# Performance work log

Measured on AMD Instinct MI355X. Metric: run time of the kernel, lower is better.

The kernel has to match this reference:

```python
import jax, jax.numpy as jnp
import numpy as np

N = 50000          # nodes
E = 800000         # edges
F_IN, H, OUT = 512, 256, 2
BN_EPS = 1e-5


def setup_inputs() -> dict:
    key = jax.random.key(0)
    ks = jax.random.split(key, 10)
    x = jax.random.normal(ks[0], (N, F_IN), jnp.float32)
    edge_index = jax.random.randint(ks[1], (2, E), 0, N, dtype=jnp.int64)
    edge_weight = jax.random.uniform(ks[2], (E,), jnp.float32)

    def lin(k, fan_in, fan_out):
        return jax.random.normal(k, (fan_in, fan_out), jnp.float32) / np.sqrt(fan_in).astype(np.float32)

    W1, b1 = lin(ks[3], F_IN, H), jnp.zeros((H,), jnp.float32)
    W2, b2 = lin(ks[4], H, H), jnp.zeros((H,), jnp.float32)
    W3, b3 = lin(ks[5], H, OUT), jnp.zeros((OUT,), jnp.float32)
    # BatchNorm1d affine params + running stats (eval mode)
    g1, be1 = jnp.ones((H,), jnp.float32), jnp.zeros((H,), jnp.float32)
    m1 = 0.1 * jax.random.normal(ks[6], (H,), jnp.float32)
    v1 = jax.random.uniform(ks[7], (H,), jnp.float32, 0.5, 1.5)
    g2, be2 = jnp.ones((H,), jnp.float32), jnp.zeros((H,), jnp.float32)
    m2 = 0.1 * jax.random.normal(ks[8], (H,), jnp.float32)
    v2 = jax.random.uniform(ks[9], (H,), jnp.float32, 0.5, 1.5)
    return {"x": x, "edge_index": edge_index, "edge_weight": edge_weight,
            "W1": W1, "b1": b1, "g1": g1, "be1": be1, "m1": m1, "v1": v1,
            "W2": W2, "b2": b2, "g2": g2, "be2": be2, "m2": m2, "v2": v2,
            "W3": W3, "b3": b3}


def gcn_conv(x, row, col, w, W, b):
    # PyG GCNConv (eval): h = x @ W; out[col] += norm * h[row]; + b
    # row/col/w already include self-loops with weight 1.
    n = x.shape[0]
    h = x @ W                                      # [N, out]
    deg = jax.ops.segment_sum(w, col, num_segments=n)
    dinv = jnp.where(deg > 0, jax.lax.rsqrt(deg), 0.0)
    norm = dinv[row] * w * dinv[col]               # [E+N]
    out = jax.ops.segment_sum(h[row] * norm[:, None], col, num_segments=n)
    return out + b


def batchnorm_eval(x, g, be, m, v):
    return (x - m) * jax.lax.rsqrt(v + BN_EPS) * g + be


def reference(x, edge_index, edge_weight, W1, b1, g1, be1, m1, v1,
              W2, b2, g2, be2, m2, v2, W3, b3):
    n = x.shape[0]
    loops = jnp.arange(n, dtype=edge_index.dtype)
    row = jnp.concatenate([edge_index[0], loops])
    col = jnp.concatenate([edge_index[1], loops])
    w = jnp.concatenate([edge_weight, jnp.ones((n,), x.dtype)])

    h = jax.nn.relu(batchnorm_eval(gcn_conv(x, row, col, w, W1, b1), g1, be1, m1, v1))
    h = jax.nn.relu(batchnorm_eval(gcn_conv(h, row, col, w, W2, b2), g2, be2, m2, v2))
    return gcn_conv(h, row, col, w, W3, b3)
```

## Files before the change

kernel.cpp:

```cpp
#include <hip/hip_runtime.h>
#include <stdint.h>

#define F_IN 512
#define HF 256
#define OUT_F 2
#define BN_EPS 1e-5f
#define SCAN_B 256
#define LDSTR 36

typedef __attribute__((ext_vector_type(8))) short bf16x8;
typedef __attribute__((ext_vector_type(4))) float f32x4;

__device__ inline float bf2f(unsigned short u) {
    union { float f; uint32_t i; } v; v.i = ((uint32_t)u) << 16; return v.f;
}
__device__ inline unsigned short f2bf(float f) {
    union { float f; uint32_t i; } v; v.f = f;
    uint32_t r = v.i + 0x7FFFu + ((v.i >> 16) & 1u);
    return (unsigned short)(r >> 16);
}

__global__ void count_conv_kernel(const int* __restrict__ col,
                                  const float* __restrict__ w,
                                  unsigned long long* __restrict__ packed,
                                  const float* __restrict__ x,
                                  unsigned short* __restrict__ xbf,
                                  const float* __restrict__ W1, unsigned short* __restrict__ W1t,
                                  const float* __restrict__ W2, unsigned short* __restrict__ W2t,
                                  unsigned short* __restrict__ xbf_pad,
                                  unsigned short* __restrict__ bufa_pad,
                                  int e, int nchunk, int padx, int pada) {
    int tid = blockIdx.x * blockDim.x + threadIdx.x;
    const int stride = gridDim.x * blockDim.x;
    if (tid < e) {
        unsigned long long add = (1ULL << 40)
            | (unsigned long long)__float2uint_rn(w[tid] * 1048576.0f);
        atomicAdd(&packed[col[tid]], add);
    }
    const float4* x4 = (const float4*)x;
    for (int c = tid; c < nchunk; c += stride) {
        float4 f0 = x4[2 * c];
        float4 f1 = x4[2 * c + 1];
        bf16x8 v;
        v[0] = (short)f2bf(f0.x); v[1] = (short)f2bf(f0.y);
        v[2] = (short)f2bf(f0.z); v[3] = (short)f2bf(f0.w);
        v[4] = (short)f2bf(f1.x); v[5] = (short)f2bf(f1.y);
        v[6] = (short)f2bf(f1.z); v[7] = (short)f2bf(f1.w);
        *(bf16x8*)(xbf + (size_t)c * 8) = v;
    }
    for (int j = tid; j < F_IN * HF; j += stride) {
        int nn = j >> 9, k = j & (F_IN - 1);
        W1t[j] = f2bf(W1[(size_t)k * HF + nn]);
    }
    for (int j = tid; j < HF * HF; j += stride) {
        int nn = j >> 8, k = j & (HF - 1);
        W2t[j] = f2bf(W2[(size_t)k * HF + nn]);
    }
    for (int j = tid; j < padx; j += stride) xbf_pad[j] = 0;
    for (int j = tid; j < pada; j += stride) bufa_pad[j] = 0;
}

__global__ void scan1_kernel(const unsigned long long* __restrict__ packed,
                             int* __restrict__ local, int* __restrict__ blocksum, int n) {
    __shared__ int tmp[SCAN_B];
    int i = blockIdx.x * SCAN_B + threadIdx.x;
    int v = (i < n) ? (int)(packed[i] >> 40) : 0;
    tmp[threadIdx.x] = v;
    __syncthreads();
    for (int off = 1; off < SCAN_B; off <<= 1) {
        int t = 0;
        if ((int)threadIdx.x >= off) t = tmp[threadIdx.x - off];
        __syncthreads();
        if ((int)threadIdx.x >= off) tmp[threadIdx.x] += t;
        __syncthreads();
    }
    if (i < n) local[i] = tmp[threadIdx.x] - v;
    if (threadIdx.x == SCAN_B - 1) blocksum[blockIdx.x] = tmp[SCAN_B - 1];
}

__global__ void scan3_dinv_kernel(int* __restrict__ csr_ptr, int* __restrict__ cursor,
                                  const int* __restrict__ blocksum,
                                  const unsigned long long* __restrict__ packed,
                                  float* __restrict__ dinv, int n, int e, int nb) {
    __shared__ int red[SCAN_B];
    int t = threadIdx.x;
    red[t] = (t < nb && t < (int)blockIdx.x) ? blocksum[t] : 0;
    __syncthreads();
    for (int off = SCAN_B / 2; off > 0; off >>= 1) {
        if (t < off) red[t] += red[t + off];
        __syncthreads();
    }
    int prefix = red[0];
    int i = blockIdx.x * SCAN_B + t;
    if (i < n) {
        int val = csr_ptr[i] + prefix;
        csr_ptr[i] = val;
        cursor[i] = val;
        float deg = 1.0f + (float)(packed[i] & 0xFFFFFFFFFFULL) * (1.0f / 1048576.0f);
        dinv[i] = rsqrtf(deg);
    }
    if (i == 0) csr_ptr[n] = e;
}

__device__ __forceinline__
void gemm_body(const unsigned short* __restrict__ A,
               const unsigned short* __restrict__ Bt,
               unsigned short* __restrict__ C, int K, int mblk, int nblk,
               unsigned short (*As)[128 * LDSTR], unsigned short (*Bs)[128 * LDSTR]) {
    const int tid  = threadIdx.x;
    const int lane = tid & 63;
    const int wv   = tid >> 6;
    const int wrow = wv >> 1, wcol = wv & 1;
    const int m0 = mblk * 128;
    const int n0 = nblk * 128;

    const int sr = tid >> 2;
    const int sc = (tid & 3) * 8;

    const unsigned short* pa0 = A + (size_t)(m0 + sr) * K + sc;
    const unsigned short* pa1 = A + (size_t)(m0 + sr + 64) * K + sc;
    const unsigned short* pb0 = Bt + (size_t)(n0 + sr) * K + sc;
    const unsigned short* pb1 = Bt + (size_t)(n0 + sr + 64) * K + sc;

    f32x4 zero4 = {0.0f, 0.0f, 0.0f, 0.0f};
    f32x4 acc[4][4];
    #pragma unroll
    for (int i = 0; i < 4; ++i)
        #pragma unroll
        for (int j = 0; j < 4; ++j) acc[i][j] = zero4;

    const int q8 = (lane >> 4) * 8;
    const int ml = lane & 15;

    bf16x8 va0 = *(const bf16x8*)pa0;
    bf16x8 va1 = *(const bf16x8*)pa1;
    bf16x8 vb0 = *(const bf16x8*)pb0;
    bf16x8 vb1 = *(const bf16x8*)pb1;

    const int nsteps = K >> 5;
    for (int s = 0; s < nsteps; ++s) {
        const int buf = s & 1;
        *(bf16x8*)&As[buf][sr * LDSTR + sc]        = va0;
        *(bf16x8*)&As[buf][(sr + 64) * LDSTR + sc] = va1;
        *(bf16x8*)&Bs[buf][sr * LDSTR + sc]        = vb0;
        *(bf16x8*)&Bs[buf][(sr + 64) * LDSTR + sc] = vb1;
        __syncthreads();
        if (s + 1 < nsteps) {
            int off = (s + 1) * 32;
            va0 = *(const bf16x8*)(pa0 + off);
            va1 = *(const bf16x8*)(pa1 + off);
            vb0 = *(const bf16x8*)(pb0 + off);
            vb1 = *(const bf16x8*)(pb1 + off);
        }
        bf16x8 af[4], bfr[4];
        #pragma unroll
        for (int i = 0; i < 4; ++i)
            af[i] = *(const bf16x8*)&As[buf][(wrow * 64 + i * 16 + ml) * LDSTR + q8];
        #pragma unroll
        for (int j = 0; j < 4; ++j)
            bfr[j] = *(const bf16x8*)&Bs[buf][(wcol * 64 + j * 16 + ml) * LDSTR + q8];
        #pragma unroll
        for (int i = 0; i < 4; ++i)
            #pragma unroll
            for (int j = 0; j < 4; ++j)
                acc[i][j] = __builtin_amdgcn_mfma_f32_16x16x32_bf16(af[i], bfr[j], acc[i][j], 0, 0, 0);
    }

    const int q4 = (lane >> 4) * 4;
    #pragma unroll
    for (int i = 0; i < 4; ++i) {
        #pragma unroll
        for (int j = 0; j < 4; ++j) {
            #pragma unroll
            for (int rg = 0; rg < 4; ++rg) {
                int r = m0 + wrow * 64 + i * 16 + q4 + rg;
                int c = n0 + wcol * 64 + j * 16 + ml;
                C[(size_t)r * HF + c] = f2bf(acc[i][j][rg]);
            }
        }
    }
}

__global__ __launch_bounds__(256)
void fill_gemm1_kernel(const int* __restrict__ row, const int* __restrict__ col,
                       const float* __restrict__ w, const float* __restrict__ dinv,
                       int* __restrict__ cursor, int2* __restrict__ csr_edge, int e,
                       const unsigned short* __restrict__ A,
                       const unsigned short* __restrict__ Bt,
                       unsigned short* __restrict__ C, int nfill) {
    __shared__ unsigned short As[2][128 * LDSTR];
    __shared__ unsigned short Bs[2][128 * LDSTR];
    int bid = blockIdx.x;
    if (bid < nfill) {
        int i = bid * 256 + (int)threadIdx.x;
        if (i < e) {
            int r = row[i], c = col[i];
            int pos = atomicAdd(&cursor[c], 1);
            float nrm = dinv[r] * w[i] * dinv[c];
            csr_edge[pos] = make_int2(r, __float_as_int(nrm));
        }
    } else {
        int gb = bid - nfill;
        gemm_body(A, Bt, C, F_IN, gb >> 1, gb & 1, As, Bs);
    }
}

__global__ __launch_bounds__(256)
void gemm_kernel(const unsigned short* __restrict__ A,
                 const unsigned short* __restrict__ Bt,
                 unsigned short* __restrict__ C, int K) {
    __shared__ unsigned short As[2][128 * LDSTR];
    __shared__ unsigned short Bs[2][128 * LDSTR];
    gemm_body(A, Bt, C, K, blockIdx.x, blockIdx.y, As, Bs);
}

template<int FINAL>
__global__ void agg_kernel(const unsigned short* __restrict__ h,
                           const int* __restrict__ ptr,
                           const int2* __restrict__ edge,
                           const float* __restrict__ dinv,
                           const float* __restrict__ b, const float* __restrict__ g,
                           const float* __restrict__ be, const float* __restrict__ m,
                           const float* __restrict__ v,
                           unsigned short* __restrict__ out,
                           const float* __restrict__ W3, float* __restrict__ h3, int n) {
    int wid  = (blockIdx.x * blockDim.x + threadIdx.x) >> 6;
    int lane = threadIdx.x & 63;
    if (wid >= n) return;
    int p0 = ptr[wid], p1 = ptr[wid + 1];
    const int fo = lane * 4;
    float a0 = 0.f, a1 = 0.f, a2 = 0.f, a3 = 0.f;

    const int cnt = p1 - p0;
    const int nb  = cnt >> 3;

    int2 edC[8], edN[8];
    ushort4 hvC[8];

    if (nb > 0) {
        #pragma unroll
        for (int k = 0; k < 8; ++k) edC[k] = edge[p0 + k];
        if (nb > 1) {
            #pragma unroll
            for (int k = 0; k < 8; ++k) edN[k] = edge[p0 + 8 + k];
        }
        #pragma unroll
        for (int k = 0; k < 8; ++k)
            hvC[k] = *(const ushort4*)(h + (size_t)edC[k].x * HF + fo);

        for (int bb = 0; bb < nb; ++bb) {
            ushort4 hvN[8];
            int2 edN2[8];
            if (bb + 1 < nb) {
                if (bb + 2 < nb) {
                    int pp = p0 + (bb + 2) * 8;
                    #pragma unroll
                    for (int k = 0; k < 8; ++k) edN2[k] = edge[pp + k];
                }
                #pragma unroll
                for (int k = 0; k < 8; ++k)
                    hvN[k] = *(const ushort4*)(h + (size_t)edN[k].x * HF + fo);
            }
            #pragma unroll
            for (int k = 0; k < 8; ++k) {
                float nw = __int_as_float(edC[k].y);
                a0 += nw * bf2f(hvC[k].x);
                a1 += nw * bf2f(hvC[k].y);
                a2 += nw * bf2f(hvC[k].z);
                a3 += nw * bf2f(hvC[k].w);
            }
            #pragma unroll
            for (int k = 0; k < 8; ++k) { edC[k] = edN[k]; edN[k] = edN2[k]; hvC[k] = hvN[k]; }
        }
    }
    const int pend = p0 + nb * 8;
    if (pend < p1) {
        int2 ed[8];
        float wv[8];
        #pragma unroll
        for (int k = 0; k < 8; ++k) {
            int idx = pend + k < p1 ? pend + k : p1 - 1;
            ed[k] = edge[idx];
            wv[k] = (pend + k < p1) ? __int_as_float(ed[k].y) : 0.0f;
        }
        ushort4 hv[8];
        #pragma unroll
        for (int k = 0; k < 8; ++k)
            hv[k] = *(const ushort4*)(h + (size_t)ed[k].x * HF + fo);
        #pragma unroll
        for (int k = 0; k < 8; ++k) {
            a0 += wv[k] * bf2f(hv[k].x);
            a1 += wv[k] * bf2f(hv[k].y);
            a2 += wv[k] * bf2f(hv[k].z);
            a3 += wv[k] * bf2f(hv[k].w);
        }
    }
    float s = dinv[wid];
    float sl = s * s;
    ushort4 hv = *(const ushort4*)(h + (size_t)wid * HF + fo);
    a0 += sl * bf2f(hv.x);
    a1 += sl * bf2f(hv.y);
    a2 += sl * bf2f(hv.z);
    a3 += sl * bf2f(hv.w);

    float4 bb  = *(const float4*)(b + fo);
    float4 gg  = *(const float4*)(g + fo);
    float4 bee = *(const float4*)(be + fo);
    float4 mm  = *(const float4*)(m + fo);
    float4 vv  = *(const float4*)(v + fo);
    float f0 = fmaxf((a0 + bb.x - mm.x) * rsqrtf(vv.x + BN_EPS) * gg.x + bee.x, 0.f);
    float f1 = fmaxf((a1 + bb.y - mm.y) * rsqrtf(vv.y + BN_EPS) * gg.y + bee.y, 0.f);
    float f2 = fmaxf((a2 + bb.z - mm.z) * rsqrtf(vv.z + BN_EPS) * gg.z + bee.z, 0.f);
    float f3 = fmaxf((a3 + bb.w - mm.w) * rsqrtf(vv.w + BN_EPS) * gg.w + bee.w, 0.f);

    if (!FINAL) {
        ushort4 o;
        o.x = f2bf(f0); o.y = f2bf(f1); o.z = f2bf(f2); o.w = f2bf(f3);
        *(ushort4*)(out + (size_t)wid * HF + fo) = o;
    } else {
        float4 w0 = *(const float4*)(W3 + fo * 2);
        float4 w1 = *(const float4*)(W3 + fo * 2 + 4);
        float s0 = f0 * w0.x + f1 * w0.z + f2 * w1.x + f3 * w1.z;
        float s1 = f0 * w0.y + f1 * w0.w + f2 * w1.y + f3 * w1.w;
        #pragma unroll
        for (int o = 32; o > 0; o >>= 1) {
            s0 += __shfl_down(s0, o, 64);
            s1 += __shfl_down(s1, o, 64);
        }
        if (lane == 0) {
            h3[wid * 2 + 0] = s0;
            h3[wid * 2 + 1] = s1;
        }
    }
}

__global__ void out_kernel(const float* __restrict__ h3,
                           const int* __restrict__ ptr, const int2* __restrict__ edge,
                           const float* __restrict__ dinv,
                           const float* __restrict__ b3, float* __restrict__ out, int n) {
    int i = blockIdx.x * blockDim.x + threadIdx.x;
    if (i >= n) return;
    int p0 = ptr[i], p1 = ptr[i + 1];
    float a0 = 0.f, a1 = 0.f;
    for (int p = p0; p < p1; p += 4) {
        #pragma unroll
        for (int k = 0; k < 4; ++k) {
            int idx = p + k < p1 ? p + k : p1 - 1;
            int2 e = edge[idx];
            float nw = (p + k < p1) ? __int_as_float(e.y) : 0.0f;
            float2 u = *(const float2*)(h3 + 2 * e.x);
            a0 += nw * u.x;
            a1 += nw * u.y;
        }
    }
    float s = dinv[i];
    float sl = s * s;
    out[2 * i + 0] = a0 + sl * h3[2 * i + 0] + b3[0];
    out[2 * i + 1] = a1 + sl * h3[2 * i + 1] + b3[1];
}

static inline char* align16(char* p) {
    return (char*)(((uintptr_t)p + 15) & ~(uintptr_t)15);
}

extern "C" void kernel_launch(void* const* d_in, const int* in_sizes, int n_in,
                              void* d_out, int out_size, void* d_ws, size_t ws_size,
                              hipStream_t stream) {
    const float* x   = (const float*)d_in[0];
    const int*   ei  = (const int*)d_in[1];
    const float* ew  = (const float*)d_in[2];
    const float* W1  = (const float*)d_in[3];
    const float* b1  = (const float*)d_in[4];
    const float* g1  = (const float*)d_in[5];
    const float* be1 = (const float*)d_in[6];
    const float* m1  = (const float*)d_in[7];
    const float* v1  = (const float*)d_in[8];
    const float* W2  = (const float*)d_in[9];
    const float* b2  = (const float*)d_in[10];
    const float* g2  = (const float*)d_in[11];
    const float* be2 = (const float*)d_in[12];
    const float* m2  = (const float*)d_in[13];
    const float* v2  = (const float*)d_in[14];
    const float* W3  = (const float*)d_in[15];
    const float* b3  = (const float*)d_in[16];

    const int N  = in_sizes[0] / F_IN;
    const int E  = in_sizes[2];
    const int MP = (N + 127) & ~127;
    const int* row = ei;
    const int* col = ei + E;

    char* wsb = (char*)d_ws;
    unsigned long long* packed = (unsigned long long*)wsb; wsb = align16(wsb + (size_t)N * 8);
    float* dinv     = (float*)wsb;          wsb = align16(wsb + (size_t)N * 4);
    int*   csr_ptr  = (int*)wsb;            wsb = align16(wsb + (size_t)(N + 1) * 4);
    int*   cursor   = (int*)wsb;            wsb = align16(wsb + (size_t)N * 4);
    int*   blocksum = (int*)wsb;            wsb = align16(wsb + (size_t)SCAN_B * 4);
    int2*  csr_edge = (int2*)wsb;           wsb = align16(wsb + (size_t)E * 8);
    unsigned short* W1t = (unsigned short*)wsb;  wsb = align16(wsb + (size_t)F_IN * HF * 2);
    unsigned short* W2t = (unsigned short*)wsb;  wsb = align16(wsb + (size_t)HF * HF * 2);
    unsigned short* xbf  = (unsigned short*)wsb; wsb = align16(wsb + (size_t)MP * F_IN * 2);
    unsigned short* bufh = (unsigned short*)wsb; wsb = align16(wsb + (size_t)MP * HF * 2);
    unsigned short* bufa = (unsigned short*)wsb; wsb = align16(wsb + (size_t)MP * HF * 2);
    float* h3 = (float*)wsb;                wsb = align16(wsb + (size_t)N * OUT_F * 4);
    float* outf = (float*)d_out;

    const int TB = 256;
    const int nscan = (N + SCAN_B - 1) / SCAN_B;
    const int padx = (MP - N) * F_IN;
    const int pada = (MP - N) * HF;
    const int ncc = (E + TB - 1) / TB;
    const int nchunk = (N * F_IN) / 8;
    const int nfill = (E + TB - 1) / TB;
    const int ngemm = (MP / 128) * 2;

    hipMemsetAsync(packed, 0, (size_t)N * 8, stream);

    count_conv_kernel<<<ncc, TB, 0, stream>>>(
        col, ew, packed, x, xbf, W1, W1t, W2, W2t,
        xbf + (size_t)N * F_IN, bufa + (size_t)N * HF, E, nchunk, padx, pada);

    scan1_kernel<<<nscan, SCAN_B, 0, stream>>>(packed, csr_ptr, blocksum, N);
    scan3_dinv_kernel<<<nscan, SCAN_B, 0, stream>>>(csr_ptr, cursor, blocksum, packed, dinv, N, E, nscan);

    fill_gemm1_kernel<<<nfill + ngemm, TB, 0, stream>>>(
        row, col, ew, dinv, cursor, csr_edge, E, xbf, W1t, bufh, nfill);

    agg_kernel<0><<<((size_t)N * 64 + TB - 1) / TB, TB, 0, stream>>>(
        bufh, csr_ptr, csr_edge, dinv, b1, g1, be1, m1, v1, bufa, nullptr, nullptr, N);

    dim3 ggrid(MP / 128, HF / 128);
    gemm_kernel<<<ggrid, TB, 0, stream>>>(bufa, W2t, bufh, HF);

    agg_kernel<1><<<((size_t)N * 64 + TB - 1) / TB, TB, 0, stream>>>(
        bufh, csr_ptr, csr_edge, dinv, b2, g2, be2, m2, v2, nullptr, W3, h3, N);

    out_kernel<<<(N + TB - 1) / TB, TB, 0, stream>>>(h3, csr_ptr, csr_edge, dinv, b3, outf, N);
}
```

Before: 533.3 us.

## Fuse two-pass scan into one kernel with grid barrier; cap fill blocks

Merges the block-local scan and prefix-add/dinv kernels into a single kernel. Each block publishes its partial sum and then spin-waits on an atomic counter until all blocks have done so. This removes one kernel launch and the csr_ptr round-trip, but depends on all ~196 blocks being co-resident to avoid deadlock. Separately, the CSR fill part of the fused fill+GEMM1 kernel now uses 512 blocks with a grid-stride loop instead of one block per 256 edges, which shrinks the grid.

```diff
diff --git a/kernel.cpp b/kernel.cpp
--- a/kernel.cpp
+++ b/kernel.cpp
@@ -60,40 +60,44 @@
     for (int j = tid; j < pada; j += stride) bufa_pad[j] = 0;
 }
 
-__global__ void scan1_kernel(const unsigned long long* __restrict__ packed,
-                             int* __restrict__ local, int* __restrict__ blocksum, int n) {
+__global__ void scan_kernel(const unsigned long long* __restrict__ packed,
+                            int* __restrict__ csr_ptr, int* __restrict__ cursor,
+                            float* __restrict__ dinv,
+                            int* __restrict__ partial, int* __restrict__ counter,
+                            int n, int e, int nb) {
     __shared__ int tmp[SCAN_B];
-    int i = blockIdx.x * SCAN_B + threadIdx.x;
+    const int tid = threadIdx.x;
+    const int bid = blockIdx.x;
+    int i = bid * SCAN_B + tid;
     int v = (i < n) ? (int)(packed[i] >> 40) : 0;
-    tmp[threadIdx.x] = v;
+    tmp[tid] = v;
     __syncthreads();
     for (int off = 1; off < SCAN_B; off <<= 1) {
         int t = 0;
-        if ((int)threadIdx.x >= off) t = tmp[threadIdx.x - off];
+        if (tid >= off) t = tmp[tid - off];
         __syncthreads();
-        if ((int)threadIdx.x >= off) tmp[threadIdx.x] += t;
+        if (tid >= off) tmp[tid] += t;
         __syncthreads();
     }
-    if (i < n) local[i] = tmp[threadIdx.x] - v;
-    if (threadIdx.x == SCAN_B - 1) blocksum[blockIdx.x] = tmp[SCAN_B - 1];
-}
-
-__global__ void scan3_dinv_kernel(int* __restrict__ csr_ptr, int* __restrict__ cursor,
-                                  const int* __restrict__ blocksum,
-                                  const unsigned long long* __restrict__ packed,
-                                  float* __restrict__ dinv, int n, int e, int nb) {
-    __shared__ int red[SCAN_B];
-    int t = threadIdx.x;
-    red[t] = (t < nb && t < (int)blockIdx.x) ? blocksum[t] : 0;
+    int excl = tmp[tid] - v;
+    if (tid == SCAN_B - 1) {
+        partial[bid] = tmp[SCAN_B - 1];
+        __threadfence();
+        atomicAdd(counter, 1);
+    }
+    if (tid == 0) {
+        while (__hip_atomic_load(counter, __ATOMIC_ACQUIRE, __HIP_MEMORY_SCOPE_AGENT) < nb) {}
+    }
+    __syncthreads();
+    tmp[tid] = (tid < nb && tid < bid) ? partial[tid] : 0;
     __syncthreads();
     for (int off = SCAN_B / 2; off > 0; off >>= 1) {
-        if (t < off) red[t] += red[t + off];
+        if (tid < off) tmp[tid] += tmp[tid + off];
         __syncthreads();
     }
-    int prefix = red[0];
-    int i = blockIdx.x * SCAN_B + t;
+    int prefix = tmp[0];
     if (i < n) {
-        int val = csr_ptr[i] + prefix;
+        int val = excl + prefix;
         csr_ptr[i] = val;
         cursor[i] = val;
         float deg = 1.0f + (float)(packed[i] & 0xFFFFFFFFFFULL) * (1.0f / 1048576.0f);
@@ -192,8 +196,8 @@
     __shared__ unsigned short Bs[2][128 * LDSTR];
     int bid = blockIdx.x;
     if (bid < nfill) {
-        int i = bid * 256 + (int)threadIdx.x;
-        if (i < e) {
+        const int stride = nfill * 256;
+        for (int i = bid * 256 + (int)threadIdx.x; i < e; i += stride) {
             int r = row[i], c = col[i];
             int pos = atomicAdd(&cursor[c], 1);
             float nrm = dinv[r] * w[i] * dinv[c];
@@ -391,11 +395,12 @@
     const int* col = ei + E;
 
     char* wsb = (char*)d_ws;
-    unsigned long long* packed = (unsigned long long*)wsb; wsb = align16(wsb + (size_t)N * 8);
+    unsigned long long* packed = (unsigned long long*)wsb; wsb = align16(wsb + (size_t)(N + 2) * 8);
+    int* counter    = (int*)(packed + N);
     float* dinv     = (float*)wsb;          wsb = align16(wsb + (size_t)N * 4);
     int*   csr_ptr  = (int*)wsb;            wsb = align16(wsb + (size_t)(N + 1) * 4);
     int*   cursor   = (int*)wsb;            wsb = align16(wsb + (size_t)N * 4);
-    int*   blocksum = (int*)wsb;            wsb = align16(wsb + (size_t)SCAN_B * 4);
+    int*   partial  = (int*)wsb;            wsb = align16(wsb + (size_t)SCAN_B * 4);
     int2*  csr_edge = (int2*)wsb;           wsb = align16(wsb + (size_t)E * 8);
     unsigned short* W1t = (unsigned short*)wsb;  wsb = align16(wsb + (size_t)F_IN * HF * 2);
     unsigned short* W2t = (unsigned short*)wsb;  wsb = align16(wsb + (size_t)HF * HF * 2);
@@ -411,17 +416,17 @@
     const int pada = (MP - N) * HF;
     const int ncc = (E + TB - 1) / TB;
     const int nchunk = (N * F_IN) / 8;
-    const int nfill = (E + TB - 1) / TB;
+    const int nfill = 512;
     const int ngemm = (MP / 128) * 2;
 
-    hipMemsetAsync(packed, 0, (size_t)N * 8, stream);
+    hipMemsetAsync(packed, 0, (size_t)(N + 2) * 8, stream);
 
     count_conv_kernel<<<ncc, TB, 0, stream>>>(
         col, ew, packed, x, xbf, W1, W1t, W2, W2t,
         xbf + (size_t)N * F_IN, bufa + (size_t)N * HF, E, nchunk, padx, pada);
 
-    scan1_kernel<<<nscan, SCAN_B, 0, stream>>>(packed, csr_ptr, blocksum, N);
-    scan3_dinv_kernel<<<nscan, SCAN_B, 0, stream>>>(csr_ptr, cursor, blocksum, packed, dinv, N, E, nscan);
+    scan_kernel<<<nscan, SCAN_B, 0, stream>>>(packed, csr_ptr, cursor, dinv,
+                                              partial, counter, N, E, nscan);
 
     fill_gemm1_kernel<<<nfill + ngemm, TB, 0, stream>>>(
         row, col, ew, dinv, cursor, csr_edge, E, xbf, W1t, bufh, nfill);
```

Measured after the change: 528.9 us. Within noise of the previous version (-0.8%).
